# Performance work log

Measured on AMD Instinct MI355X. Metric: run time of the kernel, lower is better.

Reference implementation:

```python
import jax, jax.numpy as jnp
import numpy as np

N_HEAD = 8
D_MODEL = 512
D_K = 512
D_V = 512
D_KH = D_K // N_HEAD
D_VH = D_V // N_HEAD
EPS = 1e-6


def setup_inputs() -> dict:
    key = jax.random.key(0)
    ks = jax.random.split(key, 10)
    B, L = 16, 1024
    q = jax.random.normal(ks[0], (B, L, D_MODEL), dtype=jnp.float32)
    k = jax.random.normal(ks[1], (B, L, D_MODEL), dtype=jnp.float32)
    v = jax.random.normal(ks[2], (B, L, D_MODEL), dtype=jnp.float32)
    mask = jax.random.randint(ks[3], (B, L, L), 0, 2).astype(bool)
    s = 1.0 / np.sqrt(D_MODEL)
    Wq = jax.random.normal(ks[4], (D_MODEL, D_K), dtype=jnp.float32) * s
    Wk = jax.random.normal(ks[5], (D_MODEL, D_K), dtype=jnp.float32) * s
    Wv = jax.random.normal(ks[6], (D_MODEL, D_V), dtype=jnp.float32) * s
    Wfc = jax.random.normal(ks[7], (D_V, D_MODEL), dtype=jnp.float32) * (1.0 / np.sqrt(D_V))
    gamma = jnp.ones((D_MODEL,), dtype=jnp.float32)
    beta = jnp.zeros((D_MODEL,), dtype=jnp.float32)
    return {"q": q, "k": k, "v": v, "mask": mask, "Wq": Wq, "Wk": Wk,
            "Wv": Wv, "Wfc": Wfc, "gamma": gamma, "beta": beta}


def reference(q, k, v, mask, Wq, Wk, Wv, Wfc, gamma, beta):
    B, Lq, _ = q.shape
    Lk = k.shape[1]
    residual = q
    # projections -> [B, H, L, d_head]
    qh = (q @ Wq).reshape(B, Lq, N_HEAD, D_KH).transpose(0, 2, 1, 3)
    kh = (k @ Wk).reshape(B, Lk, N_HEAD, D_KH).transpose(0, 2, 1, 3)
    vh = (v @ Wv).reshape(B, Lk, N_HEAD, D_VH).transpose(0, 2, 1, 3)
    # scaled dot-product attention; scale uses per-head dim (source rebinds d_k)
    scores = jnp.einsum('bhqd,bhkd->bhqk', qh / np.sqrt(D_KH), kh)
    scores = jnp.where(mask[:, None, :, :], -1e9, scores)
    attn = jax.nn.softmax(scores, axis=-1)
    out = jnp.einsum('bhqk,bhkd->bhqd', attn, vh)
    out = out.transpose(0, 2, 1, 3).reshape(B, Lq, D_V)
    out = out @ Wfc + residual
    # layer norm
    mu = jnp.mean(out, axis=-1, keepdims=True)
    var = jnp.var(out, axis=-1, keepdims=True)
    out = (out - mu) * jax.lax.rsqrt(var + EPS) * gamma + beta
    return out, attn
```

## Files before the change

kernel.cpp:

```cpp
#include <hip/hip_runtime.h>
#include <hip/hip_bf16.h>

typedef __attribute__((ext_vector_type(8))) short s8v;
typedef __attribute__((ext_vector_type(4))) short s4v;
typedef __attribute__((ext_vector_type(4))) float f4v;

__device__ __forceinline__ short f2bf(float f){
  unsigned u = __builtin_bit_cast(unsigned, f);
  u += 0x7fffu + ((u >> 16) & 1u);
  return (short)(u >> 16);
}

__device__ __forceinline__ f4v mfma16(s8v a, s8v b, f4v c){
  return __builtin_amdgcn_mfma_f32_16x16x32_bf16(a, b, c, 0, 0, 0);
}

__global__ __launch_bounds__(256) void prep_kernel(
    const int* __restrict__ mask, unsigned* __restrict__ bits,
    const float* __restrict__ Wq, const float* __restrict__ Wk,
    const float* __restrict__ Wv, const float* __restrict__ Wfc,
    short* __restrict__ Wt)
{
  if (blockIdx.x < 2048){
    const int lane = threadIdx.x & 63;
    const int wid = blockIdx.x*4 + (threadIdx.x >> 6);
    for (int i = 0; i < 32; ++i){
      const int c = wid*32 + i;
      int mv = __builtin_nontemporal_load(&mask[(size_t)c*64 + lane]);
      unsigned long long bal = __ballot(mv != 0);
      if (lane == 0)  bits[c*2]   = (unsigned)bal;
      if (lane == 32) bits[c*2+1] = (unsigned)(bal >> 32);
    }
  } else {
    const int bid = blockIdx.x - 2048;
    const int w = bid >> 10;
    const float* __restrict__ W = (w==0)?Wq:(w==1)?Wk:(w==2)?Wv:Wfc;
    const int idx = (bid & 1023)*256 + threadIdx.x;
    const int kk = idx >> 9, n = idx & 511;
    Wt[w*262144 + n*512 + kk] = f2bf(W[idx]);
  }
}

__global__ __launch_bounds__(256) void proj_kernel(
    const float* __restrict__ qin, const float* __restrict__ kin,
    const float* __restrict__ vin, const short* __restrict__ Wt,
    short* __restrict__ Qh, short* __restrict__ Kh, short* __restrict__ Vt)
{
  const int work = (blockIdx.x & 7)*384 + (blockIdx.x >> 3);
  const int z = work >> 10;
  const int r = work & 1023;
  const int mt = r >> 2, nt = r & 3;
  const float* __restrict__ A = (z==0) ? qin : (z==1) ? kin : vin;
  const short* __restrict__ W = Wt + z*262144;
  const int m0 = mt*64, n0 = nt*128;
  __shared__ __align__(16) short Alds[64*40];
  const int tid = threadIdx.x, lane = tid & 63, wave = tid >> 6;
  const int wm = wave >> 1, wn = wave & 1;
  const int col = lane & 15, kg = lane >> 4;
  f4v acc[2][4];
  #pragma unroll
  for (int i=0;i<2;i++)
    #pragma unroll
    for (int j=0;j<4;j++) acc[i][j] = (f4v){0.f,0.f,0.f,0.f};

  const int arow = tid >> 2, aoff = (tid & 3)*8;
  const float* Ap = A + (size_t)(m0 + arow)*512 + aoff;
  short* Aw = &Alds[arow*40 + aoff];

  for (int k0 = 0; k0 < 512; k0 += 32){
    float4 x0 = *(const float4*)(Ap + k0);
    float4 x1 = *(const float4*)(Ap + k0 + 4);
    s8v ab;
    ab[0]=f2bf(x0.x); ab[1]=f2bf(x0.y); ab[2]=f2bf(x0.z); ab[3]=f2bf(x0.w);
    ab[4]=f2bf(x1.x); ab[5]=f2bf(x1.y); ab[6]=f2bf(x1.z); ab[7]=f2bf(x1.w);
    __syncthreads();
    *(s8v*)Aw = ab;
    __syncthreads();
    s8v af0 = *(const s8v*)&Alds[(wm*32 + col)*40 + kg*8];
    s8v af1 = *(const s8v*)&Alds[(wm*32 + 16 + col)*40 + kg*8];
    #pragma unroll
    for (int f=0; f<4; f++){
      const int n = n0 + wn*64 + f*16 + col;
      s8v bf = *(const s8v*)(W + n*512 + k0 + kg*8);
      acc[0][f] = mfma16(af0, bf, acc[0][f]);
      acc[1][f] = mfma16(af1, bf, acc[1][f]);
    }
  }
  const float scale = (z==0) ? 0.125f : 1.0f;
  #pragma unroll
  for (int fr=0; fr<2; fr++)
    #pragma unroll
    for (int f=0; f<4; f++)
      #pragma unroll
      for (int j=0; j<4; j++){
        int rr = m0 + wm*32 + fr*16 + kg*4 + j;
        int c = n0 + wn*64 + f*16 + col;
        int b = rr >> 10, l = rr & 1023, hh = c >> 6, d = c & 63;
        short val = f2bf(acc[fr][f][j] * scale);
        if (z==0)      Qh[((size_t)(b*8+hh)*1024 + l)*64 + d] = val;
        else if (z==1) Kh[((size_t)(b*8+hh)*1024 + l)*64 + d] = val;
        else           Vt[((size_t)(b*8+hh)*64 + d)*1024 + l] = val;
      }
}

__global__ __launch_bounds__(256) void attn_kernel(
  const short* __restrict__ Qh, const short* __restrict__ Kh,
  const short* __restrict__ Vt, const unsigned* __restrict__ bits,
  float* __restrict__ attn, short* __restrict__ ctx)
{
  const int work = ((blockIdx.x & 7) << 8) | (blockIdx.x >> 3);
  const int bh = work >> 4;
  const int q0 = (work & 15) * 64;
  const int b = bh >> 3, h = bh & 7;
  __shared__ unsigned mb[64*33];
  __shared__ __align__(16) short Pb[64*128];
  __shared__ float red[256];
  __shared__ float rowinv[64];
  const int tid = threadIdx.x, lane = tid & 63, wave = tid >> 6;
  const int col = lane & 15, kg = lane >> 4;
  const short* Qb = Qh + (size_t)bh*65536;
  const short* Kb = Kh + (size_t)bh*65536;
  const short* Vb = Vt + (size_t)bh*65536;
  const f4v zf = (f4v){0.f,0.f,0.f,0.f};

  {
    const int r = tid >> 2, w = (tid & 3)*8;
    const unsigned* src = bits + (size_t)(b*1024 + q0 + r)*32 + w;
    uint4 w0 = *(const uint4*)src;
    uint4 w1 = *(const uint4*)(src + 4);
    unsigned* dst = &mb[r*33 + w];
    dst[0]=w0.x; dst[1]=w0.y; dst[2]=w0.z; dst[3]=w0.w;
    dst[4]=w1.x; dst[5]=w1.y; dst[6]=w1.z; dst[7]=w1.w;
  }

  s8v qf[4][2];
  #pragma unroll
  for (int qi = 0; qi < 4; ++qi)
    #pragma unroll
    for (int ks = 0; ks < 2; ++ks)
      qf[qi][ks] = *(const s8v*)(Qb + (q0 + qi*16 + col)*64 + ks*32 + kg*8);

  __syncthreads();

  float sum[4] = {0.f, 0.f, 0.f, 0.f};
  for (int it = 0; it < 8; ++it){
    const int c0 = it*128 + wave*32;
    unsigned mw[4];
    #pragma unroll
    for (int qi = 0; qi < 4; ++qi) mw[qi] = mb[(qi*16 + col)*33 + (c0>>5)];
    #pragma unroll
    for (int ch = 0; ch < 2; ++ch){
      const short* kp = Kb + (c0 + ch*16 + col)*64 + kg*8;
      s8v kf0 = *(const s8v*)kp;
      s8v kf1 = *(const s8v*)(kp + 32);
      #pragma unroll
      for (int qi = 0; qi < 4; ++qi){
        f4v a = mfma16(kf0, qf[qi][0], zf);
        a = mfma16(kf1, qf[qi][1], a);
        #pragma unroll
        for (int j = 0; j < 4; ++j){
          const int bit = ch*16 + kg*4 + j;
          float e = __expf(a[j]);
          sum[qi] += ((mw[qi]>>bit)&1) ? 0.f : e;
        }
      }
    }
  }
  #pragma unroll
  for (int qi = 0; qi < 4; ++qi){
    sum[qi] += __shfl_xor(sum[qi], 16);
    sum[qi] += __shfl_xor(sum[qi], 32);
  }
  if (kg == 0){
    #pragma unroll
    for (int qi = 0; qi < 4; ++qi) red[wave*64 + qi*16 + col] = sum[qi];
  }
  __syncthreads();
  if (tid < 64)
    rowinv[tid] = 1.0f / (red[tid] + red[64+tid] + red[128+tid] + red[192+tid]);
  __syncthreads();
  float inv[4];
  #pragma unroll
  for (int qi = 0; qi < 4; ++qi) inv[qi] = rowinv[qi*16 + col];

  f4v cacc[4] = {zf, zf, zf, zf};
  const int d0 = wave*16;
  float* ab = attn + (size_t)(bh*1024 + q0)*1024;
  const int sw = (col & 7) << 3;
  for (int it = 0; it < 8; ++it){
    const int c0 = it*128 + wave*32;
    unsigned mw[4];
    #pragma unroll
    for (int qi = 0; qi < 4; ++qi) mw[qi] = mb[(qi*16 + col)*33 + (c0>>5)];
    #pragma unroll
    for (int ch = 0; ch < 2; ++ch){
      const int cc = c0 + ch*16;
      const short* kp = Kb + (cc + col)*64 + kg*8;
      s8v kf0 = *(const s8v*)kp;
      s8v kf1 = *(const s8v*)(kp + 32);
      #pragma unroll
      for (int qi = 0; qi < 4; ++qi){
        f4v a = mfma16(kf0, qf[qi][0], zf);
        a = mfma16(kf1, qf[qi][1], a);
        f4v p; s4v pk;
        #pragma unroll
        for (int j = 0; j < 4; ++j){
          const int bit = ch*16 + kg*4 + j;
          float e = __expf(a[j]) * inv[qi];
          p[j] = ((mw[qi]>>bit)&1) ? 0.f : e;
          pk[j] = f2bf(p[j]);
        }
        __builtin_nontemporal_store(p,
            (f4v*)(ab + (size_t)(qi*16 + col)*1024 + cc + kg*4));
        *(s4v*)&Pb[(qi*16 + col)*128 + ((wave*32 + ch*16 + kg*4) ^ sw)] = pk;
      }
    }
    __syncthreads();
    #pragma unroll
    for (int sub = 0; sub < 4; ++sub){
      s8v vf = *(const s8v*)(Vb + (size_t)(d0 + col)*1024 + it*128 + sub*32 + kg*8);
      const int kr = (sub*32 + kg*8) ^ sw;
      #pragma unroll
      for (int qi = 0; qi < 4; ++qi){
        s8v pa = *(const s8v*)&Pb[(qi*16 + col)*128 + kr];
        cacc[qi] = mfma16(pa, vf, cacc[qi]);
      }
    }
    __syncthreads();
  }

  short* cb = ctx + (size_t)(b*1024 + q0)*512 + h*64 + d0 + col;
  #pragma unroll
  for (int qi = 0; qi < 4; ++qi)
    #pragma unroll
    for (int j = 0; j < 4; ++j)
      cb[(size_t)(qi*16 + kg*4 + j)*512] = f2bf(cacc[qi][j]);
}

__global__ __launch_bounds__(256) void outproj_ln_kernel(
  const short* __restrict__ ctx, const short* __restrict__ Wf,
  const float* __restrict__ resid, const float* __restrict__ gamma,
  const float* __restrict__ beta, float* __restrict__ out)
{
  const int m0 = blockIdx.x * 32;
  __shared__ __align__(16) short Alds[32*40];
  __shared__ float sred[32*4], qred[32*4];
  __shared__ float mLds[32], rLds[32];
  const int tid = threadIdx.x, lane = tid & 63, wave = tid >> 6;
  const int col = lane & 15, kg = lane >> 4;
  const int n0 = wave * 128;

  f4v acc[2][8];
  #pragma unroll
  for (int mf=0; mf<2; mf++)
    #pragma unroll
    for (int nf=0; nf<8; nf++) acc[mf][nf] = (f4v){0.f,0.f,0.f,0.f};

  const int arow = tid >> 3, ac = (tid & 7)*4;
  const short* Ap = ctx + (size_t)(m0 + arow)*512 + ac;
  short* Aw = &Alds[arow*40 + ac];

  for (int k0 = 0; k0 < 512; k0 += 32){
    s4v av = *(const s4v*)(Ap + k0);
    __syncthreads();
    *(s4v*)Aw = av;
    __syncthreads();
    s8v af[2];
    #pragma unroll
    for (int mf=0; mf<2; mf++)
      af[mf] = *(const s8v*)&Alds[(mf*16 + col)*40 + kg*8];
    #pragma unroll
    for (int nf=0; nf<8; nf++){
      s8v bf = *(const s8v*)(Wf + (size_t)(n0 + nf*16 + col)*512 + k0 + kg*8);
      #pragma unroll
      for (int mf=0; mf<2; mf++)
        acc[mf][nf] = mfma16(af[mf], bf, acc[mf][nf]);
    }
  }

  float g[8], bt[8];
  #pragma unroll
  for (int nf=0; nf<8; nf++){
    g[nf]  = gamma[n0 + nf*16 + col];
    bt[nf] = beta[n0 + nf*16 + col];
  }

  #pragma unroll
  for (int mf=0; mf<2; mf++)
    #pragma unroll
    for (int j=0; j<4; j++){
      const int rl = mf*16 + kg*4 + j;
      const size_t r = (size_t)(m0 + rl);
      float s = 0.f, qq = 0.f;
      #pragma unroll
      for (int nf=0; nf<8; nf++){
        float y = acc[mf][nf][j] + resid[r*512 + n0 + nf*16 + col];
        acc[mf][nf][j] = y;
        s += y; qq += y*y;
      }
      #pragma unroll
      for (int d=1; d<16; d<<=1){ s += __shfl_xor(s, d); qq += __shfl_xor(qq, d); }
      if (col == 0){ sred[rl*4 + wave] = s; qred[rl*4 + wave] = qq; }
    }
  __syncthreads();
  if (tid < 32){
    float S = sred[tid*4] + sred[tid*4+1] + sred[tid*4+2] + sred[tid*4+3];
    float Q = qred[tid*4] + qred[tid*4+1] + qred[tid*4+2] + qred[tid*4+3];
    float mean = S * (1.0f/512.0f);
    float var  = Q * (1.0f/512.0f) - mean*mean;
    mLds[tid] = mean;
    rLds[tid] = rsqrtf(var + 1e-6f);
  }
  __syncthreads();

  #pragma unroll
  for (int mf=0; mf<2; mf++)
    #pragma unroll
    for (int j=0; j<4; j++){
      const int rl = mf*16 + kg*4 + j;
      const size_t r = (size_t)(m0 + rl);
      const float mean = mLds[rl], rs = rLds[rl];
      #pragma unroll
      for (int nf=0; nf<8; nf++)
        out[r*512 + n0 + nf*16 + col] = (acc[mf][nf][j] - mean)*rs*g[nf] + bt[nf];
    }
}

extern "C" void kernel_launch(void* const* d_in, const int* in_sizes, int n_in,
                              void* d_out, int out_size, void* d_ws, size_t ws_size,
                              hipStream_t stream) {
  const float* q    = (const float*)d_in[0];
  const float* k    = (const float*)d_in[1];
  const float* v    = (const float*)d_in[2];
  const int*   mask = (const int*)d_in[3];
  const float* Wq   = (const float*)d_in[4];
  const float* Wk   = (const float*)d_in[5];
  const float* Wv   = (const float*)d_in[6];
  const float* Wfc  = (const float*)d_in[7];
  const float* gamma= (const float*)d_in[8];
  const float* beta = (const float*)d_in[9];

  char* ws = (char*)d_ws;
  short* Wt  = (short*)(ws);
  short* Qh  = (short*)(ws + ((size_t)2<<20));
  short* Kh  = (short*)(ws + ((size_t)18<<20));
  short* Vt  = (short*)(ws + ((size_t)34<<20));
  short* ctx = (short*)(ws + ((size_t)50<<20));

  float* out  = (float*)d_out;
  float* attn = out + (size_t)16384*512;
  unsigned* bits = (unsigned*)d_out;

  prep_kernel<<<dim3(6144,1,1), 256, 0, stream>>>(mask, bits, Wq, Wk, Wv, Wfc, Wt);
  proj_kernel <<<dim3(3072,1,1), 256, 0, stream>>>(q, k, v, Wt, Qh, Kh, Vt);
  attn_kernel <<<dim3(2048,1,1), 256, 0, stream>>>(Qh, Kh, Vt, bits, attn, ctx);
  outproj_ln_kernel<<<dim3(512,1,1), 256, 0, stream>>>(ctx, Wt + 3*262144, q,
                                                       gamma, beta, out);
}
```

Measured before the change: 394.5 us.

## Prefetch next A tile, use LDS-only barriers, and stage V transpose through LDS

The projection and output-projection GEMM loops now issue the next k-step's global loads before the barrier, so load latency overlaps the current MFMA work. __syncthreads is replaced by a barrier that waits only on LDS counters, so outstanding global loads do not stall it. The V projection epilogue now transposes its tile through shared memory and writes 16-byte coalesced rows to Vt, replacing the strided 2-byte scattered stores. This adds extra LDS for the transpose buffer, which may lower occupancy of the projection kernel.

```diff
diff --git a/kernel.cpp b/kernel.cpp
--- a/kernel.cpp
+++ b/kernel.cpp
@@ -13,6 +13,12 @@
 
 __device__ __forceinline__ f4v mfma16(s8v a, s8v b, f4v c){
   return __builtin_amdgcn_mfma_f32_16x16x32_bf16(a, b, c, 0, 0, 0);
+}
+
+__device__ __forceinline__ void ldsbar(){
+  asm volatile("s_waitcnt lgkmcnt(0)" ::: "memory");
+  __builtin_amdgcn_s_barrier();
+  __builtin_amdgcn_sched_barrier(0);
 }
 
 __global__ __launch_bounds__(256) void prep_kernel(
@@ -54,6 +60,7 @@
   const short* __restrict__ W = Wt + z*262144;
   const int m0 = mt*64, n0 = nt*128;
   __shared__ __align__(16) short Alds[64*40];
+  __shared__ __align__(16) short Tlds[128*68];
   const int tid = threadIdx.x, lane = tid & 63, wave = tid >> 6;
   const int wm = wave >> 1, wn = wave & 1;
   const int col = lane & 15, kg = lane >> 4;
@@ -67,15 +74,20 @@
   const float* Ap = A + (size_t)(m0 + arow)*512 + aoff;
   short* Aw = &Alds[arow*40 + aoff];
 
+  float4 x0 = *(const float4*)(Ap);
+  float4 x1 = *(const float4*)(Ap + 4);
+
   for (int k0 = 0; k0 < 512; k0 += 32){
-    float4 x0 = *(const float4*)(Ap + k0);
-    float4 x1 = *(const float4*)(Ap + k0 + 4);
     s8v ab;
     ab[0]=f2bf(x0.x); ab[1]=f2bf(x0.y); ab[2]=f2bf(x0.z); ab[3]=f2bf(x0.w);
     ab[4]=f2bf(x1.x); ab[5]=f2bf(x1.y); ab[6]=f2bf(x1.z); ab[7]=f2bf(x1.w);
-    __syncthreads();
+    ldsbar();
     *(s8v*)Aw = ab;
-    __syncthreads();
+    if (k0 < 480){
+      x0 = *(const float4*)(Ap + k0 + 32);
+      x1 = *(const float4*)(Ap + k0 + 36);
+    }
+    ldsbar();
     s8v af0 = *(const s8v*)&Alds[(wm*32 + col)*40 + kg*8];
     s8v af1 = *(const s8v*)&Alds[(wm*32 + 16 + col)*40 + kg*8];
     #pragma unroll
@@ -86,21 +98,44 @@
       acc[1][f] = mfma16(af1, bf, acc[1][f]);
     }
   }
-  const float scale = (z==0) ? 0.125f : 1.0f;
-  #pragma unroll
-  for (int fr=0; fr<2; fr++)
-    #pragma unroll
-    for (int f=0; f<4; f++)
-      #pragma unroll
-      for (int j=0; j<4; j++){
-        int rr = m0 + wm*32 + fr*16 + kg*4 + j;
-        int c = n0 + wn*64 + f*16 + col;
-        int b = rr >> 10, l = rr & 1023, hh = c >> 6, d = c & 63;
-        short val = f2bf(acc[fr][f][j] * scale);
-        if (z==0)      Qh[((size_t)(b*8+hh)*1024 + l)*64 + d] = val;
-        else if (z==1) Kh[((size_t)(b*8+hh)*1024 + l)*64 + d] = val;
-        else           Vt[((size_t)(b*8+hh)*64 + d)*1024 + l] = val;
-      }
+
+  if (z < 2){
+    const float scale = (z==0) ? 0.125f : 1.0f;
+    short* D = (z==0) ? Qh : Kh;
+    #pragma unroll
+    for (int fr=0; fr<2; fr++)
+      #pragma unroll
+      for (int f=0; f<4; f++)
+        #pragma unroll
+        for (int j=0; j<4; j++){
+          int rr = m0 + wm*32 + fr*16 + kg*4 + j;
+          int c = n0 + wn*64 + f*16 + col;
+          int b = rr >> 10, l = rr & 1023, hh = c >> 6, d = c & 63;
+          D[((size_t)(b*8+hh)*1024 + l)*64 + d] = f2bf(acc[fr][f][j] * scale);
+        }
+  } else {
+    ldsbar();
+    #pragma unroll
+    for (int fr=0; fr<2; fr++)
+      #pragma unroll
+      for (int f=0; f<4; f++)
+        #pragma unroll
+        for (int j=0; j<4; j++){
+          const int rl = wm*32 + fr*16 + kg*4 + j;
+          const int cl = wn*64 + f*16 + col;
+          Tlds[cl*68 + rl] = f2bf(acc[fr][f][j]);
+        }
+    ldsbar();
+    const int b = m0 >> 10, lbase = m0 & 1023;
+    #pragma unroll
+    for (int it=0; it<4; ++it){
+      const int idx = it*256 + tid;
+      const int cl = idx >> 3, rc = idx & 7;
+      const int c = n0 + cl, hh = c >> 6, d = c & 63;
+      s8v vv = *(const s8v*)&Tlds[cl*68 + rc*8];
+      *(s8v*)(Vt + ((size_t)(b*8+hh)*64 + d)*1024 + lbase + rc*8) = vv;
+    }
+  }
 }
 
 __global__ __launch_bounds__(256) void attn_kernel(
@@ -215,7 +250,7 @@
         *(s4v*)&Pb[(qi*16 + col)*128 + ((wave*32 + ch*16 + kg*4) ^ sw)] = pk;
       }
     }
-    __syncthreads();
+    ldsbar();
     #pragma unroll
     for (int sub = 0; sub < 4; ++sub){
       s8v vf = *(const s8v*)(Vb + (size_t)(d0 + col)*1024 + it*128 + sub*32 + kg*8);
@@ -226,7 +261,7 @@
         cacc[qi] = mfma16(pa, vf, cacc[qi]);
       }
     }
-    __syncthreads();
+    ldsbar();
   }
 
   short* cb = ctx + (size_t)(b*1024 + q0)*512 + h*64 + d0 + col;
@@ -260,11 +295,13 @@
   const short* Ap = ctx + (size_t)(m0 + arow)*512 + ac;
   short* Aw = &Alds[arow*40 + ac];
 
+  s4v av = *(const s4v*)(Ap);
+
   for (int k0 = 0; k0 < 512; k0 += 32){
-    s4v av = *(const s4v*)(Ap + k0);
-    __syncthreads();
+    ldsbar();
     *(s4v*)Aw = av;
-    __syncthreads();
+    if (k0 < 480) av = *(const s4v*)(Ap + k0 + 32);
+    ldsbar();
     s8v af[2];
     #pragma unroll
     for (int mf=0; mf<2; mf++)
```

Result: faster. 355.9 us (-9.8%).
